# Kernel tuning notes

Measured on AMD Instinct MI355X. Metric: run time of the kernel, lower is better.

The kernel has to match this reference:

```python
import jax, jax.numpy as jnp
import numpy as np

EMBED_DIM = 768
NUM_HEADS = 12
HEAD_DIM = EMBED_DIM // NUM_HEADS


def setup_inputs() -> dict:
    key = jax.random.key(0)
    ks = jax.random.split(key, 9)
    s = 1.0 / np.sqrt(EMBED_DIM)
    inp = {
        "x": jax.random.normal(ks[0], (4, 2048, EMBED_DIM), dtype=jnp.float32),
        "W_q": jax.random.uniform(ks[1], (EMBED_DIM, EMBED_DIM), jnp.float32, -s, s),
        "b_q": jax.random.uniform(ks[2], (EMBED_DIM,), jnp.float32, -s, s),
        "W_k": jax.random.uniform(ks[3], (EMBED_DIM, EMBED_DIM), jnp.float32, -s, s),
        "b_k": jax.random.uniform(ks[4], (EMBED_DIM,), jnp.float32, -s, s),
        "W_v": jax.random.uniform(ks[5], (EMBED_DIM, EMBED_DIM), jnp.float32, -s, s),
        "b_v": jax.random.uniform(ks[6], (EMBED_DIM,), jnp.float32, -s, s),
        "W_out": jax.random.uniform(ks[7], (EMBED_DIM, EMBED_DIM), jnp.float32, -s, s),
        "b_out": jax.random.uniform(ks[8], (EMBED_DIM,), jnp.float32, -s, s),
    }
    return inp


def reference(x, W_q, b_q, W_k, b_k, W_v, b_v, W_out, b_out):
    B, N, D = x.shape
    H, Hd = NUM_HEADS, HEAD_DIM
    scale = 1.0 / jnp.sqrt(jnp.asarray(Hd, x.dtype))
    # QKV projections (torch Linear: x @ W.T + b)
    Q = (x @ W_q.T + b_q).reshape(B, N, H, Hd).transpose(0, 2, 1, 3)  # (B,H,N,Hd)
    K = (x @ W_k.T + b_k).reshape(B, N, H, Hd).transpose(0, 2, 1, 3)
    V = (x @ W_v.T + b_v).reshape(B, N, H, Hd).transpose(0, 2, 1, 3)
    scores = jnp.einsum("bhqd,bhkd->bhqk", Q, K) * scale  # (B,H,N,N)
    attn = jax.nn.softmax(scores, axis=-1)
    out = jnp.einsum("bhqk,bhkd->bhqd", attn, V)  # (B,H,N,Hd)
    out = out.transpose(0, 2, 1, 3).reshape(B, N, D)
    return out @ W_out.T + b_out
```

## Files before the change

### kernel.cpp

```cpp
#include <hip/hip_runtime.h>
#include <math.h>

#define D_EMB 768
#define SEQN 2048
#define NB 4
#define NH 12
#define HDIM 64
#define MTOT (NB*SEQN)
#define SCLQ 0.18033688011112042f

typedef unsigned int u32;
typedef unsigned short u16;
typedef short sh4 __attribute__((ext_vector_type(4)));
typedef short bf16x8 __attribute__((ext_vector_type(8)));
typedef float f32x16 __attribute__((ext_vector_type(16)));

#define MFMA32(a,b,c) __builtin_amdgcn_mfma_f32_32x32x16_bf16((a),(b),(c),0,0,0)

__device__ __forceinline__ u32 cvtpk(float a, float b){
    u32 r; asm("v_cvt_pk_bf16_f32 %0, %1, %2" : "=v"(r) : "v"(a), "v"(b)); return r;
}
__device__ __forceinline__ u32 pack_split(float v){
    u32 h = cvtpk(v, v);
    float hf = __builtin_bit_cast(float, h << 16);
    float r = v - hf;
    u32 l = cvtpk(r, r);
    return __builtin_amdgcn_perm(l, h, 0x05040100u);
}
__device__ __forceinline__ void unpack4(uint4 p, sh4& hi, sh4& lo){
    u32 h0 = __builtin_amdgcn_perm(p.y, p.x, 0x05040100u);
    u32 h1 = __builtin_amdgcn_perm(p.w, p.z, 0x05040100u);
    u32 l0 = __builtin_amdgcn_perm(p.y, p.x, 0x07060302u);
    u32 l1 = __builtin_amdgcn_perm(p.w, p.z, 0x07060302u);
    uint2 h = {h0, h1}, l = {l0, l1};
    hi = __builtin_bit_cast(sh4, h);
    lo = __builtin_bit_cast(sh4, l);
}
__device__ __forceinline__ bf16x8 ldfrag(const short* p){
    sh4 a = *(const sh4*)p;
    sh4 b = *(const sh4*)(p+4);
    return __builtin_shufflevector(a,b,0,1,2,3,4,5,6,7);
}

__global__ __launch_bounds__(256) void pack_bf(const float* __restrict__ s, u16* __restrict__ d, int n4){
    int i = blockIdx.x*256 + threadIdx.x;
    if (i >= n4) return;
    float4 v = ((const float4*)s)[i];
    uint2 o = { cvtpk(v.x, v.y), cvtpk(v.z, v.w) };
    ((uint2*)d)[i] = o;
}
__global__ __launch_bounds__(256) void pack_wbf(const float* __restrict__ w0, const float* __restrict__ w1,
                                                const float* __restrict__ w2, const float* __restrict__ w3,
                                                u16* __restrict__ d, int n4){
    const int z = blockIdx.y;
    const float* s = (z==0)?w0:(z==1)?w1:(z==2)?w2:w3;
    int i = blockIdx.x*256 + threadIdx.x;
    if (i >= n4) return;
    float4 v = ((const float4*)s)[i];
    uint2 o = { cvtpk(v.x, v.y), cvtpk(v.z, v.w) };
    ((uint2*)(d + (size_t)z*n4*4))[i] = o;
}

#define GPAD 36

__global__ __launch_bounds__(256,3) void gemm_qkv(const u16* __restrict__ X, const u16* __restrict__ Wb,
        const float* __restrict__ bq, const float* __restrict__ bk, const float* __restrict__ bv,
        u16* __restrict__ oq, u16* __restrict__ okk, u16* __restrict__ ov){
    __shared__ __align__(16) short Ahi[128][GPAD];
    __shared__ __align__(16) short Bhi[128][GPAD];

    const int tid = threadIdx.x;
    const int l = tid & 63, w = tid >> 6;
    const int lq = l & 31, g = l >> 5;
    const int wm = w >> 1, wn = w & 1;
    const int m0 = blockIdx.x * 128;
    const int n0 = blockIdx.y * 128;
    const int z  = blockIdx.z;
    const u16* W = Wb + (size_t)z * D_EMB * D_EMB;
    const float* bias = (z==0) ? bq : (z==1) ? bk : bv;
    u16* out = (z==0) ? oq : (z==1) ? okk : ov;

    f32x16 acc[2][2];
    #pragma unroll
    for (int i=0;i<2;i++)
        #pragma unroll
        for (int j=0;j<2;j++)
            #pragma unroll
            for (int r=0;r<16;r++) acc[i][j][r] = 0.f;

    const int srow = tid >> 1;
    const int skb  = (tid & 1) * 16;
    const u16* ap0 = X + (size_t)(m0+srow)*D_EMB + skb;
    const u16* wp0 = W + (size_t)(n0+srow)*D_EMB + skb;

    uint4 a0 = *(const uint4*)ap0, a1 = *(const uint4*)(ap0+8);
    uint4 w0 = *(const uint4*)wp0, w1 = *(const uint4*)(wp0+8);

    for (int k0 = 0; k0 < D_EMB; k0 += 32) {
        __syncthreads();
        {
            uint2 t;
            t.x=a0.x; t.y=a0.y; *(uint2*)&Ahi[srow][skb]    = t;
            t.x=a0.z; t.y=a0.w; *(uint2*)&Ahi[srow][skb+4]  = t;
            t.x=a1.x; t.y=a1.y; *(uint2*)&Ahi[srow][skb+8]  = t;
            t.x=a1.z; t.y=a1.w; *(uint2*)&Ahi[srow][skb+12] = t;
            t.x=w0.x; t.y=w0.y; *(uint2*)&Bhi[srow][skb]    = t;
            t.x=w0.z; t.y=w0.w; *(uint2*)&Bhi[srow][skb+4]  = t;
            t.x=w1.x; t.y=w1.y; *(uint2*)&Bhi[srow][skb+8]  = t;
            t.x=w1.z; t.y=w1.w; *(uint2*)&Bhi[srow][skb+12] = t;
        }
        if (k0 + 32 < D_EMB){
            const u16* ap = ap0 + k0 + 32;
            const u16* wp = wp0 + k0 + 32;
            a0 = *(const uint4*)ap; a1 = *(const uint4*)(ap+8);
            w0 = *(const uint4*)wp; w1 = *(const uint4*)(wp+8);
        }
        __syncthreads();
        #pragma unroll
        for (int kk=0;kk<2;kk++){
            const int kc = kk*16 + g*8;
            bf16x8 ah[2], bh[2];
            #pragma unroll
            for (int i=0;i<2;i++) ah[i] = ldfrag(&Ahi[wm*64+32*i+lq][kc]);
            #pragma unroll
            for (int j=0;j<2;j++) bh[j] = ldfrag(&Bhi[wn*64+32*j+lq][kc]);
            #pragma unroll
            for (int i=0;i<2;i++)
                #pragma unroll
                for (int j=0;j<2;j++)
                    acc[i][j] = MFMA32(ah[i], bh[j], acc[i][j]);
        }
    }

    #pragma unroll
    for (int j=0;j<2;j++){
        const int c = n0 + wn*64 + 32*j + lq;
        const float bv2 = bias[c];
        #pragma unroll
        for (int i=0;i<2;i++){
            #pragma unroll
            for (int r=0;r<16;r++){
                const int m = m0 + wm*64 + 32*i + (r&3) + 8*(r>>2) + 4*g;
                float v = acc[i][j][r] + bv2;
                if (z==0) v *= SCLQ;
                const int b = m >> 11, n = m & 2047, h = c >> 6, hd = c & 63;
                out[(((size_t)(b*NH + h))*SEQN + n)*HDIM + hd] = (u16)cvtpk(v, v);
            }
        }
    }
}

__global__ __launch_bounds__(256,3) void gemm_out(const u32* __restrict__ A, const u16* __restrict__ Wb,
        const float* __restrict__ bo, float* __restrict__ outp){
    __shared__ __align__(16) short Ahi[128][GPAD];
    __shared__ __align__(16) short Alo[128][GPAD];
    __shared__ __align__(16) short Bhi[128][GPAD];

    const int tid = threadIdx.x;
    const int l = tid & 63, w = tid >> 6;
    const int lq = l & 31, g = l >> 5;
    const int wm = w >> 1, wn = w & 1;
    const int m0 = blockIdx.x * 128;
    const int n0 = blockIdx.y * 128;
    const u16* W = Wb + (size_t)3 * D_EMB * D_EMB;

    f32x16 acc[2][2];
    #pragma unroll
    for (int i=0;i<2;i++)
        #pragma unroll
        for (int j=0;j<2;j++)
            #pragma unroll
            for (int r=0;r<16;r++) acc[i][j][r] = 0.f;

    const int srow = tid >> 1;
    const int skb  = (tid & 1) * 16;
    const u32* ap0 = A + (size_t)(m0+srow)*D_EMB + skb;
    const u16* wp0 = W + (size_t)(n0+srow)*D_EMB + skb;

    uint4 areg[4];
    uint4 w0 = *(const uint4*)wp0, w1 = *(const uint4*)(wp0+8);
    #pragma unroll
    for (int c=0;c<4;c++) areg[c] = *(const uint4*)(ap0 + 4*c);

    for (int k0 = 0; k0 < D_EMB; k0 += 32) {
        __syncthreads();
        #pragma unroll
        for (int c=0;c<4;c++){
            sh4 h, lo2; unpack4(areg[c], h, lo2);
            *(sh4*)&Ahi[srow][skb+4*c] = h;
            *(sh4*)&Alo[srow][skb+4*c] = lo2;
        }
        {
            uint2 t;
            t.x=w0.x; t.y=w0.y; *(uint2*)&Bhi[srow][skb]    = t;
            t.x=w0.z; t.y=w0.w; *(uint2*)&Bhi[srow][skb+4]  = t;
            t.x=w1.x; t.y=w1.y; *(uint2*)&Bhi[srow][skb+8]  = t;
            t.x=w1.z; t.y=w1.w; *(uint2*)&Bhi[srow][skb+12] = t;
        }
        if (k0 + 32 < D_EMB){
            const u32* ap = ap0 + k0 + 32;
            const u16* wp = wp0 + k0 + 32;
            #pragma unroll
            for (int c=0;c<4;c++) areg[c] = *(const uint4*)(ap + 4*c);
            w0 = *(const uint4*)wp; w1 = *(const uint4*)(wp+8);
        }
        __syncthreads();
        #pragma unroll
        for (int kk=0;kk<2;kk++){
            const int kc = kk*16 + g*8;
            bf16x8 ah[2], al[2], bh[2];
            #pragma unroll
            for (int i=0;i<2;i++){
                ah[i] = ldfrag(&Ahi[wm*64+32*i+lq][kc]);
                al[i] = ldfrag(&Alo[wm*64+32*i+lq][kc]);
            }
            #pragma unroll
            for (int j=0;j<2;j++) bh[j] = ldfrag(&Bhi[wn*64+32*j+lq][kc]);
            #pragma unroll
            for (int i=0;i<2;i++)
                #pragma unroll
                for (int j=0;j<2;j++){
                    acc[i][j] = MFMA32(ah[i], bh[j], acc[i][j]);
                    acc[i][j] = MFMA32(al[i], bh[j], acc[i][j]);
                }
        }
    }

    #pragma unroll
    for (int j=0;j<2;j++){
        const int c = n0 + wn*64 + 32*j + lq;
        const float bv2 = bo[c];
        #pragma unroll
        for (int i=0;i<2;i++){
            #pragma unroll
            for (int r=0;r<16;r++){
                const int m = m0 + wm*64 + 32*i + (r&3) + 8*(r>>2) + 4*g;
                outp[(size_t)m*D_EMB + c] = acc[i][j][r] + bv2;
            }
        }
    }
}

#define KB 64
#define KPAD 68
#define NT (SEQN/KB)

__global__ __launch_bounds__(256,3) void attn_bf(const u16* __restrict__ Qg,
                                                 const u16* __restrict__ Kg,
                                                 const u16* __restrict__ Vg,
                                                 u32* __restrict__ Og) {
    __shared__ __align__(16) short Khi[2][KB][KPAD];
    __shared__ __align__(16) short Vthi[2][HDIM][KPAD];

    const int tid = threadIdx.x;
    const int l = tid & 63, w = tid >> 6;
    const int lq = l & 31, g = l >> 5;
    const int qt = blockIdx.x;
    const int bh = blockIdx.y;
    const size_t base = (size_t)bh * SEQN * HDIM;
    const int qrow = qt*128 + w*32 + lq;

    const int key = tid >> 2, dblk = (tid & 3) * 16;
    const int hd = tid & 63, kg = tid >> 6;
    const u16* kp0 = Kg + base + (size_t)key*HDIM + dblk;
    const u16* vp0 = Vg + base + (size_t)(kg*16)*HDIM + hd;

    bf16x8 qh[4];
    {
        const u16* qp = Qg + base + (size_t)qrow*HDIM;
        #pragma unroll
        for (int kk=0;kk<4;kk++){
            uint4 a = *(const uint4*)(qp + kk*16 + g*8);
            qh[kk] = __builtin_bit_cast(bf16x8, a);
        }
    }

    f32x16 o0, o1, zro;
    #pragma unroll
    for (int r=0;r<16;r++){ o0[r]=0.f; o1[r]=0.f; zro[r]=0.f; }
    float2 lr2 = {0.f, 0.f};

    uint4 kra, krb;
    u32 vt[16];

    auto loadTile = [&](int t){
        const u16* kp = kp0 + (size_t)t*KB*HDIM;
        const u16* vp = vp0 + (size_t)t*KB*HDIM;
        kra = *(const uint4*)kp;
        krb = *(const uint4*)(kp+8);
        #pragma unroll
        for (int i2=0;i2<16;i2++) vt[i2] = vp[(size_t)i2*HDIM];
    };
    auto stageWrite = [&](int cb){
        uint2 t;
        t.x=kra.x; t.y=kra.y; *(uint2*)&Khi[cb][key][dblk]    = t;
        t.x=kra.z; t.y=kra.w; *(uint2*)&Khi[cb][key][dblk+4]  = t;
        t.x=krb.x; t.y=krb.y; *(uint2*)&Khi[cb][key][dblk+8]  = t;
        t.x=krb.z; t.y=krb.w; *(uint2*)&Khi[cb][key][dblk+12] = t;
        #pragma unroll
        for (int c=0;c<4;c++){
            uint2 v2;
            v2.x = __builtin_amdgcn_perm(vt[4*c+1], vt[4*c+0], 0x05040100u);
            v2.y = __builtin_amdgcn_perm(vt[4*c+3], vt[4*c+2], 0x05040100u);
            *(uint2*)&Vthi[cb][hd][kg*16+4*c] = v2;
        }
    };

    loadTile(0);
    stageWrite(0);
    loadTile(1);

    for (int kt=0; kt<NT; kt++){
        const int cb = kt & 1;
        __syncthreads();
        if (kt+1 < NT){
            stageWrite(cb^1);
            if (kt+2 < NT) loadTile(kt+2);
        }

        f32x16 s0, s1;
        __builtin_amdgcn_s_setprio(1);
        {
            bf16x8 a0h = ldfrag(&Khi[cb][lq][0 + g*8]);
            bf16x8 a1h = ldfrag(&Khi[cb][32+lq][0 + g*8]);
            s0 = MFMA32(a0h, qh[0], zro);
            s1 = MFMA32(a1h, qh[0], zro);
        }
        #pragma unroll
        for (int kk=1;kk<4;kk++){
            const int kc = kk*16 + g*8;
            bf16x8 a0h = ldfrag(&Khi[cb][lq][kc]);
            bf16x8 a1h = ldfrag(&Khi[cb][32+lq][kc]);
            s0 = MFMA32(a0h, qh[kk], s0);
            s1 = MFMA32(a1h, qh[kk], s1);
        }
        __builtin_amdgcn_s_setprio(0);

        #pragma unroll
        for (int r=0;r<16;r++) s0[r] = __builtin_amdgcn_exp2f(s0[r]);
        #pragma unroll
        for (int r=0;r<16;r++) s1[r] = __builtin_amdgcn_exp2f(s1[r]);
        #pragma unroll
        for (int r=0;r<16;r+=2){
            float2 a = {s0[r], s0[r+1]};
            float2 b = {s1[r], s1[r+1]};
            lr2 += a;
            lr2 += b;
        }

        u32 pk0h[8], pk1h[8];
        #pragma unroll
        for (int j=0;j<8;j++){
            pk0h[j] = cvtpk(s0[2*j], s0[2*j+1]);
            pk1h[j] = cvtpk(s1[2*j], s1[2*j+1]);
        }
        u32 n0[2][4], n1[2][4];
        #pragma unroll
        for (int a2=0;a2<2;a2++){
            #pragma unroll
            for (int c=0;c<2;c++){
                u32 x0 = pk0h[4*a2+c], y0 = pk0h[4*a2+2+c];
                asm("v_permlane32_swap_b32 %0, %1" : "+v"(x0), "+v"(y0));
                n0[0][2*a2+c] = x0; n1[0][2*a2+c] = y0;
                u32 x1 = pk1h[4*a2+c], y1 = pk1h[4*a2+2+c];
                asm("v_permlane32_swap_b32 %0, %1" : "+v"(x1), "+v"(y1));
                n0[1][2*a2+c] = x1; n1[1][2*a2+c] = y1;
            }
        }

        __builtin_amdgcn_s_setprio(1);
        #pragma unroll
        for (int kk=0;kk<4;kk++){
            const int hblk = kk>>1, a2 = kk&1;
            uint4 whv = { n0[hblk][2*a2], n0[hblk][2*a2+1], n1[hblk][2*a2], n1[hblk][2*a2+1] };
            bf16x8 pbh = __builtin_bit_cast(bf16x8, whv);
            const int kc = kk*16 + g*8;
            bf16x8 v0h = ldfrag(&Vthi[cb][lq][kc]);
            bf16x8 v1h = ldfrag(&Vthi[cb][32+lq][kc]);
            o0 = MFMA32(v0h, pbh, o0);
            o1 = MFMA32(v1h, pbh, o1);
        }
        __builtin_amdgcn_s_setprio(0);
    }

    float l_run = lr2.x + lr2.y;
    l_run += __shfl_xor(l_run, 32);
    const float inv = 1.f / l_run;
    const int b = bh / NH, h = bh % NH;
    u32* op = Og + ((size_t)(b*SEQN + qrow))*D_EMB + h*HDIM;
    #pragma unroll
    for (int rq=0; rq<4; rq++){
        uint4 w0, w1;
        w0.x = pack_split(o0[4*rq+0]*inv); w0.y = pack_split(o0[4*rq+1]*inv);
        w0.z = pack_split(o0[4*rq+2]*inv); w0.w = pack_split(o0[4*rq+3]*inv);
        w1.x = pack_split(o1[4*rq+0]*inv); w1.y = pack_split(o1[4*rq+1]*inv);
        w1.z = pack_split(o1[4*rq+2]*inv); w1.w = pack_split(o1[4*rq+3]*inv);
        *(uint4*)(op + 8*rq + 4*g)      = w0;
        *(uint4*)(op + 32 + 8*rq + 4*g) = w1;
    }
}

extern "C" void kernel_launch(void* const* d_in, const int* in_sizes, int n_in,
                              void* d_out, int out_size, void* d_ws, size_t ws_size,
                              hipStream_t stream) {
    const float* x  = (const float*)d_in[0];
    const float* Wq = (const float*)d_in[1];
    const float* bq = (const float*)d_in[2];
    const float* Wk = (const float*)d_in[3];
    const float* bk = (const float*)d_in[4];
    const float* Wv = (const float*)d_in[5];
    const float* bv = (const float*)d_in[6];
    const float* Wo = (const float*)d_in[7];
    const float* bo = (const float*)d_in[8];

    const size_t per = (size_t)NB*NH*SEQN*HDIM;
    const size_t wplane = (size_t)D_EMB*D_EMB;
    u16* base16 = (u16*)d_ws;
    u16* Xbf = base16;
    u16* Qb  = base16 + per;
    u16* Kb  = base16 + 2*per;
    u16* Vb  = base16 + 3*per;
    u16* Wbf = base16 + 4*per;
    u32* ATpk = (u32*)(base16 + 4*per + 4*wplane);

    pack_bf<<<dim3((int)(per/4/256)), dim3(256), 0, stream>>>(x, Xbf, (int)(per/4));
    pack_wbf<<<dim3(576,4), dim3(256), 0, stream>>>(Wq, Wk, Wv, Wo, Wbf, (int)(wplane/4));

    gemm_qkv<<<dim3(MTOT/128, D_EMB/128, 3), dim3(256), 0, stream>>>(Xbf, Wbf, bq, bk, bv, Qb, Kb, Vb);

    attn_bf<<<dim3(SEQN/128, NB*NH), dim3(256), 0, stream>>>(Qb, Kb, Vb, ATpk);

    gemm_out<<<dim3(MTOT/128, D_EMB/128), dim3(256), 0, stream>>>(ATpk, Wbf, bo, (float*)d_out);
}
```

Measured before the change: 156.8 us.

## Fuse fp32-to-bf16 packing into GEMMs and load K fragments directly to registers

Removes the separate pack_bf and pack_wbf kernels; the QKV and output GEMMs now load fp32 X and weights and convert to bf16 while staging into LDS. This drops two launches and a round trip of the converted tensors through global memory, at the cost of twice the global bytes per tile inside the GEMMs. Separately, the attention kernel stops staging K in LDS and loads each lane's MFMA K fragments straight from global memory into registers, prefetching the next tile after the QK MFMAs. That frees LDS and removes LDS writes and reads, but uses more registers and issues less coalesced global loads.

```diff
diff --git a/kernel.cpp b/kernel.cpp
--- a/kernel.cpp
+++ b/kernel.cpp
@@ -42,28 +42,10 @@
     return __builtin_shufflevector(a,b,0,1,2,3,4,5,6,7);
 }
 
-__global__ __launch_bounds__(256) void pack_bf(const float* __restrict__ s, u16* __restrict__ d, int n4){
-    int i = blockIdx.x*256 + threadIdx.x;
-    if (i >= n4) return;
-    float4 v = ((const float4*)s)[i];
-    uint2 o = { cvtpk(v.x, v.y), cvtpk(v.z, v.w) };
-    ((uint2*)d)[i] = o;
-}
-__global__ __launch_bounds__(256) void pack_wbf(const float* __restrict__ w0, const float* __restrict__ w1,
-                                                const float* __restrict__ w2, const float* __restrict__ w3,
-                                                u16* __restrict__ d, int n4){
-    const int z = blockIdx.y;
-    const float* s = (z==0)?w0:(z==1)?w1:(z==2)?w2:w3;
-    int i = blockIdx.x*256 + threadIdx.x;
-    if (i >= n4) return;
-    float4 v = ((const float4*)s)[i];
-    uint2 o = { cvtpk(v.x, v.y), cvtpk(v.z, v.w) };
-    ((uint2*)(d + (size_t)z*n4*4))[i] = o;
-}
-
 #define GPAD 36
 
-__global__ __launch_bounds__(256,3) void gemm_qkv(const u16* __restrict__ X, const u16* __restrict__ Wb,
+__global__ __launch_bounds__(256,3) void gemm_qkv(const float* __restrict__ X,
+        const float* __restrict__ Wq, const float* __restrict__ Wk, const float* __restrict__ Wv,
         const float* __restrict__ bq, const float* __restrict__ bk, const float* __restrict__ bv,
         u16* __restrict__ oq, u16* __restrict__ okk, u16* __restrict__ ov){
     __shared__ __align__(16) short Ahi[128][GPAD];
@@ -76,7 +58,7 @@
     const int m0 = blockIdx.x * 128;
     const int n0 = blockIdx.y * 128;
     const int z  = blockIdx.z;
-    const u16* W = Wb + (size_t)z * D_EMB * D_EMB;
+    const float* W = (z==0) ? Wq : (z==1) ? Wk : Wv;
     const float* bias = (z==0) ? bq : (z==1) ? bk : bv;
     u16* out = (z==0) ? oq : (z==1) ? okk : ov;
 
@@ -90,30 +72,28 @@
 
     const int srow = tid >> 1;
     const int skb  = (tid & 1) * 16;
-    const u16* ap0 = X + (size_t)(m0+srow)*D_EMB + skb;
-    const u16* wp0 = W + (size_t)(n0+srow)*D_EMB + skb;
-
-    uint4 a0 = *(const uint4*)ap0, a1 = *(const uint4*)(ap0+8);
-    uint4 w0 = *(const uint4*)wp0, w1 = *(const uint4*)(wp0+8);
+    const float* ap0 = X + (size_t)(m0+srow)*D_EMB + skb;
+    const float* wp0 = W + (size_t)(n0+srow)*D_EMB + skb;
+
+    float4 ar[4], wr[4];
+    #pragma unroll
+    for (int c=0;c<4;c++){ ar[c] = *(const float4*)(ap0 + 4*c); wr[c] = *(const float4*)(wp0 + 4*c); }
 
     for (int k0 = 0; k0 < D_EMB; k0 += 32) {
         __syncthreads();
-        {
+        #pragma unroll
+        for (int c=0;c<4;c++){
             uint2 t;
-            t.x=a0.x; t.y=a0.y; *(uint2*)&Ahi[srow][skb]    = t;
-            t.x=a0.z; t.y=a0.w; *(uint2*)&Ahi[srow][skb+4]  = t;
-            t.x=a1.x; t.y=a1.y; *(uint2*)&Ahi[srow][skb+8]  = t;
-            t.x=a1.z; t.y=a1.w; *(uint2*)&Ahi[srow][skb+12] = t;
-            t.x=w0.x; t.y=w0.y; *(uint2*)&Bhi[srow][skb]    = t;
-            t.x=w0.z; t.y=w0.w; *(uint2*)&Bhi[srow][skb+4]  = t;
-            t.x=w1.x; t.y=w1.y; *(uint2*)&Bhi[srow][skb+8]  = t;
-            t.x=w1.z; t.y=w1.w; *(uint2*)&Bhi[srow][skb+12] = t;
+            t.x = cvtpk(ar[c].x, ar[c].y); t.y = cvtpk(ar[c].z, ar[c].w);
+            *(uint2*)&Ahi[srow][skb+4*c] = t;
+            t.x = cvtpk(wr[c].x, wr[c].y); t.y = cvtpk(wr[c].z, wr[c].w);
+            *(uint2*)&Bhi[srow][skb+4*c] = t;
         }
         if (k0 + 32 < D_EMB){
-            const u16* ap = ap0 + k0 + 32;
-            const u16* wp = wp0 + k0 + 32;
-            a0 = *(const uint4*)ap; a1 = *(const uint4*)(ap+8);
-            w0 = *(const uint4*)wp; w1 = *(const uint4*)(wp+8);
+            const float* ap = ap0 + k0 + 32;
+            const float* wp = wp0 + k0 + 32;
+            #pragma unroll
+            for (int c=0;c<4;c++){ ar[c] = *(const float4*)(ap + 4*c); wr[c] = *(const float4*)(wp + 4*c); }
         }
         __syncthreads();
         #pragma unroll
@@ -150,7 +130,7 @@
     }
 }
 
-__global__ __launch_bounds__(256,3) void gemm_out(const u32* __restrict__ A, const u16* __restrict__ Wb,
+__global__ __launch_bounds__(256,3) void gemm_out(const u32* __restrict__ A, const float* __restrict__ Wo,
         const float* __restrict__ bo, float* __restrict__ outp){
     __shared__ __align__(16) short Ahi[128][GPAD];
     __shared__ __align__(16) short Alo[128][GPAD];
@@ -162,7 +142,6 @@
     const int wm = w >> 1, wn = w & 1;
     const int m0 = blockIdx.x * 128;
     const int n0 = blockIdx.y * 128;
-    const u16* W = Wb + (size_t)3 * D_EMB * D_EMB;
 
     f32x16 acc[2][2];
     #pragma unroll
@@ -175,12 +154,12 @@
     const int srow = tid >> 1;
     const int skb  = (tid & 1) * 16;
     const u32* ap0 = A + (size_t)(m0+srow)*D_EMB + skb;
-    const u16* wp0 = W + (size_t)(n0+srow)*D_EMB + skb;
+    const float* wp0 = Wo + (size_t)(n0+srow)*D_EMB + skb;
 
     uint4 areg[4];
-    uint4 w0 = *(const uint4*)wp0, w1 = *(const uint4*)(wp0+8);
-    #pragma unroll
-    for (int c=0;c<4;c++) areg[c] = *(const uint4*)(ap0 + 4*c);
+    float4 wr[4];
+    #pragma unroll
+    for (int c=0;c<4;c++){ areg[c] = *(const uint4*)(ap0 + 4*c); wr[c] = *(const float4*)(wp0 + 4*c); }
 
     for (int k0 = 0; k0 < D_EMB; k0 += 32) {
         __syncthreads();
@@ -189,20 +168,15 @@
             sh4 h, lo2; unpack4(areg[c], h, lo2);
             *(sh4*)&Ahi[srow][skb+4*c] = h;
             *(sh4*)&Alo[srow][skb+4*c] = lo2;
-        }
-        {
             uint2 t;
-            t.x=w0.x; t.y=w0.y; *(uint2*)&Bhi[srow][skb]    = t;
-            t.x=w0.z; t.y=w0.w; *(uint2*)&Bhi[srow][skb+4]  = t;
-            t.x=w1.x; t.y=w1.y; *(uint2*)&Bhi[srow][skb+8]  = t;
-            t.x=w1.z; t.y=w1.w; *(uint2*)&Bhi[srow][skb+12] = t;
+            t.x = cvtpk(wr[c].x, wr[c].y); t.y = cvtpk(wr[c].z, wr[c].w);
+            *(uint2*)&Bhi[srow][skb+4*c] = t;
         }
         if (k0 + 32 < D_EMB){
             const u32* ap = ap0 + k0 + 32;
-            const u16* wp = wp0 + k0 + 32;
-            #pragma unroll
-            for (int c=0;c<4;c++) areg[c] = *(const uint4*)(ap + 4*c);
-            w0 = *(const uint4*)wp; w1 = *(const uint4*)(wp+8);
+            const float* wp = wp0 + k0 + 32;
+            #pragma unroll
+            for (int c=0;c<4;c++){ areg[c] = *(const uint4*)(ap + 4*c); wr[c] = *(const float4*)(wp + 4*c); }
         }
         __syncthreads();
         #pragma unroll
@@ -249,7 +223,6 @@
                                                  const u16* __restrict__ Kg,
                                                  const u16* __restrict__ Vg,
                                                  u32* __restrict__ Og) {
-    __shared__ __align__(16) short Khi[2][KB][KPAD];
     __shared__ __align__(16) short Vthi[2][HDIM][KPAD];
 
     const int tid = threadIdx.x;
@@ -260,10 +233,9 @@
     const size_t base = (size_t)bh * SEQN * HDIM;
     const int qrow = qt*128 + w*32 + lq;
 
-    const int key = tid >> 2, dblk = (tid & 3) * 16;
     const int hd = tid & 63, kg = tid >> 6;
-    const u16* kp0 = Kg + base + (size_t)key*HDIM + dblk;
     const u16* vp0 = Vg + base + (size_t)(kg*16)*HDIM + hd;
+    const u16* kfl = Kg + base + (size_t)lq*HDIM + g*8;
 
     bf16x8 qh[4];
     {
@@ -280,23 +252,15 @@
     for (int r=0;r<16;r++){ o0[r]=0.f; o1[r]=0.f; zro[r]=0.f; }
     float2 lr2 = {0.f, 0.f};
 
-    uint4 kra, krb;
     u32 vt[16];
-
-    auto loadTile = [&](int t){
-        const u16* kp = kp0 + (size_t)t*KB*HDIM;
+    uint4 kreg[8];
+
+    auto loadV = [&](int t){
         const u16* vp = vp0 + (size_t)t*KB*HDIM;
-        kra = *(const uint4*)kp;
-        krb = *(const uint4*)(kp+8);
         #pragma unroll
         for (int i2=0;i2<16;i2++) vt[i2] = vp[(size_t)i2*HDIM];
     };
-    auto stageWrite = [&](int cb){
-        uint2 t;
-        t.x=kra.x; t.y=kra.y; *(uint2*)&Khi[cb][key][dblk]    = t;
-        t.x=kra.z; t.y=kra.w; *(uint2*)&Khi[cb][key][dblk+4]  = t;
-        t.x=krb.x; t.y=krb.y; *(uint2*)&Khi[cb][key][dblk+8]  = t;
-        t.x=krb.z; t.y=krb.w; *(uint2*)&Khi[cb][key][dblk+12] = t;
+    auto stageV = [&](int cb){
         #pragma unroll
         for (int c=0;c<4;c++){
             uint2 v2;
@@ -305,36 +269,39 @@
             *(uint2*)&Vthi[cb][hd][kg*16+4*c] = v2;
         }
     };
-
-    loadTile(0);
-    stageWrite(0);
-    loadTile(1);
+    auto loadK = [&](int t){
+        const u16* kp = kfl + (size_t)t*KB*HDIM;
+        #pragma unroll
+        for (int blk=0;blk<2;blk++)
+            #pragma unroll
+            for (int kk=0;kk<4;kk++)
+                kreg[blk*4+kk] = *(const uint4*)(kp + blk*32*HDIM + kk*16);
+    };
+
+    loadK(0);
+    loadV(0);
+    stageV(0);
+    loadV(1);
 
     for (int kt=0; kt<NT; kt++){
         const int cb = kt & 1;
         __syncthreads();
         if (kt+1 < NT){
-            stageWrite(cb^1);
-            if (kt+2 < NT) loadTile(kt+2);
+            stageV(cb^1);
+            if (kt+2 < NT) loadV(kt+2);
         }
 
         f32x16 s0, s1;
         __builtin_amdgcn_s_setprio(1);
-        {
-            bf16x8 a0h = ldfrag(&Khi[cb][lq][0 + g*8]);
-            bf16x8 a1h = ldfrag(&Khi[cb][32+lq][0 + g*8]);
-            s0 = MFMA32(a0h, qh[0], zro);
-            s1 = MFMA32(a1h, qh[0], zro);
-        }
+        s0 = MFMA32(__builtin_bit_cast(bf16x8, kreg[0]), qh[0], zro);
+        s1 = MFMA32(__builtin_bit_cast(bf16x8, kreg[4]), qh[0], zro);
         #pragma unroll
         for (int kk=1;kk<4;kk++){
-            const int kc = kk*16 + g*8;
-            bf16x8 a0h = ldfrag(&Khi[cb][lq][kc]);
-            bf16x8 a1h = ldfrag(&Khi[cb][32+lq][kc]);
-            s0 = MFMA32(a0h, qh[kk], s0);
-            s1 = MFMA32(a1h, qh[kk], s1);
+            s0 = MFMA32(__builtin_bit_cast(bf16x8, kreg[kk]),   qh[kk], s0);
+            s1 = MFMA32(__builtin_bit_cast(bf16x8, kreg[4+kk]), qh[kk], s1);
         }
         __builtin_amdgcn_s_setprio(0);
+        if (kt+1 < NT) loadK(kt+1);
 
         #pragma unroll
         for (int r=0;r<16;r++) s0[r] = __builtin_amdgcn_exp2f(s0[r]);
@@ -414,21 +381,15 @@
     const float* bo = (const float*)d_in[8];
 
     const size_t per = (size_t)NB*NH*SEQN*HDIM;
-    const size_t wplane = (size_t)D_EMB*D_EMB;
     u16* base16 = (u16*)d_ws;
-    u16* Xbf = base16;
-    u16* Qb  = base16 + per;
-    u16* Kb  = base16 + 2*per;
-    u16* Vb  = base16 + 3*per;
-    u16* Wbf = base16 + 4*per;
-    u32* ATpk = (u32*)(base16 + 4*per + 4*wplane);
-
-    pack_bf<<<dim3((int)(per/4/256)), dim3(256), 0, stream>>>(x, Xbf, (int)(per/4));
-    pack_wbf<<<dim3(576,4), dim3(256), 0, stream>>>(Wq, Wk, Wv, Wo, Wbf, (int)(wplane/4));
-
-    gemm_qkv<<<dim3(MTOT/128, D_EMB/128, 3), dim3(256), 0, stream>>>(Xbf, Wbf, bq, bk, bv, Qb, Kb, Vb);
+    u16* Qb  = base16;
+    u16* Kb  = base16 + per;
+    u16* Vb  = base16 + 2*per;
+    u32* ATpk = (u32*)(base16 + 4*per);
+
+    gemm_qkv<<<dim3(MTOT/128, D_EMB/128, 3), dim3(256), 0, stream>>>(x, Wq, Wk, Wv, bq, bk, bv, Qb, Kb, Vb);
 
     attn_bf<<<dim3(SEQN/128, NB*NH), dim3(256), 0, stream>>>(Qb, Kb, Vb, ATpk);
 
-    gemm_out<<<dim3(MTOT/128, D_EMB/128), dim3(256), 0, stream>>>(ATpk, Wbf, bo, (float*)d_out);
-}
+    gemm_out<<<dim3(MTOT/128, D_EMB/128), dim3(256), 0, stream>>>(ATpk, Wo, bo, (float*)d_out);
+}
```

Measured after the change: 204.7 us. 30.5% more time.

## Process two query tiles per wave in attention to reuse K/V fragments

Applied to the files above, without the earlier changes.

Each wave in the attention kernel now handles 64 query rows as two 32-row groups instead of one. Every K and V fragment read from LDS therefore feeds twice as many MFMAs, and the grid is halved so each block covers 256 queries. Staging K/V into shared memory is amortised over more queries, and LDS read traffic per unit of work drops. The cost is higher register pressure: launch bounds drop from 3 to 2 blocks per CU, and fewer blocks (384) are launched, which may reduce occupancy and latency hiding.

```diff
diff --git a/kernel.cpp b/kernel.cpp
--- a/kernel.cpp
+++ b/kernel.cpp
@@ -245,7 +245,7 @@
 #define KPAD 68
 #define NT (SEQN/KB)
 
-__global__ __launch_bounds__(256,3) void attn_bf(const u16* __restrict__ Qg,
+__global__ __launch_bounds__(256,2) void attn_bf(const u16* __restrict__ Qg,
                                                  const u16* __restrict__ Kg,
                                                  const u16* __restrict__ Vg,
                                                  u32* __restrict__ Og) {
@@ -258,27 +258,29 @@
     const int qt = blockIdx.x;
     const int bh = blockIdx.y;
     const size_t base = (size_t)bh * SEQN * HDIM;
-    const int qrow = qt*128 + w*32 + lq;
+    const int qrowA = qt*256 + w*64 + lq;
+    const int qrowB = qrowA + 32;
 
     const int key = tid >> 2, dblk = (tid & 3) * 16;
     const int hd = tid & 63, kg = tid >> 6;
     const u16* kp0 = Kg + base + (size_t)key*HDIM + dblk;
     const u16* vp0 = Vg + base + (size_t)(kg*16)*HDIM + hd;
 
-    bf16x8 qh[4];
+    bf16x8 qhA[4], qhB[4];
     {
-        const u16* qp = Qg + base + (size_t)qrow*HDIM;
+        const u16* qpA = Qg + base + (size_t)qrowA*HDIM;
+        const u16* qpB = Qg + base + (size_t)qrowB*HDIM;
         #pragma unroll
         for (int kk=0;kk<4;kk++){
-            uint4 a = *(const uint4*)(qp + kk*16 + g*8);
-            qh[kk] = __builtin_bit_cast(bf16x8, a);
-        }
-    }
-
-    f32x16 o0, o1, zro;
-    #pragma unroll
-    for (int r=0;r<16;r++){ o0[r]=0.f; o1[r]=0.f; zro[r]=0.f; }
-    float2 lr2 = {0.f, 0.f};
+            qhA[kk] = __builtin_bit_cast(bf16x8, *(const uint4*)(qpA + kk*16 + g*8));
+            qhB[kk] = __builtin_bit_cast(bf16x8, *(const uint4*)(qpB + kk*16 + g*8));
+        }
+    }
+
+    f32x16 oA0, oA1, oB0, oB1, zro;
+    #pragma unroll
+    for (int r=0;r<16;r++){ oA0[r]=0.f; oA1[r]=0.f; oB0[r]=0.f; oB1[r]=0.f; zro[r]=0.f; }
+    float2 lrA = {0.f, 0.f}, lrB = {0.f, 0.f};
 
     uint4 kra, krb;
     u32 vt[16];
@@ -318,85 +320,105 @@
             if (kt+2 < NT) loadTile(kt+2);
         }
 
-        f32x16 s0, s1;
-        __builtin_amdgcn_s_setprio(1);
-        {
-            bf16x8 a0h = ldfrag(&Khi[cb][lq][0 + g*8]);
-            bf16x8 a1h = ldfrag(&Khi[cb][32+lq][0 + g*8]);
-            s0 = MFMA32(a0h, qh[0], zro);
-            s1 = MFMA32(a1h, qh[0], zro);
-        }
-        #pragma unroll
-        for (int kk=1;kk<4;kk++){
-            const int kc = kk*16 + g*8;
-            bf16x8 a0h = ldfrag(&Khi[cb][lq][kc]);
-            bf16x8 a1h = ldfrag(&Khi[cb][32+lq][kc]);
-            s0 = MFMA32(a0h, qh[kk], s0);
-            s1 = MFMA32(a1h, qh[kk], s1);
-        }
-        __builtin_amdgcn_s_setprio(0);
-
-        #pragma unroll
-        for (int r=0;r<16;r++) s0[r] = __builtin_amdgcn_exp2f(s0[r]);
-        #pragma unroll
-        for (int r=0;r<16;r++) s1[r] = __builtin_amdgcn_exp2f(s1[r]);
-        #pragma unroll
-        for (int r=0;r<16;r+=2){
-            float2 a = {s0[r], s0[r+1]};
-            float2 b = {s1[r], s1[r+1]};
-            lr2 += a;
-            lr2 += b;
-        }
-
-        u32 pk0h[8], pk1h[8];
-        #pragma unroll
-        for (int j=0;j<8;j++){
-            pk0h[j] = cvtpk(s0[2*j], s0[2*j+1]);
-            pk1h[j] = cvtpk(s1[2*j], s1[2*j+1]);
-        }
-        u32 n0[2][4], n1[2][4];
-        #pragma unroll
-        for (int a2=0;a2<2;a2++){
-            #pragma unroll
-            for (int c=0;c<2;c++){
-                u32 x0 = pk0h[4*a2+c], y0 = pk0h[4*a2+2+c];
-                asm("v_permlane32_swap_b32 %0, %1" : "+v"(x0), "+v"(y0));
-                n0[0][2*a2+c] = x0; n1[0][2*a2+c] = y0;
-                u32 x1 = pk1h[4*a2+c], y1 = pk1h[4*a2+2+c];
-                asm("v_permlane32_swap_b32 %0, %1" : "+v"(x1), "+v"(y1));
-                n0[1][2*a2+c] = x1; n1[1][2*a2+c] = y1;
-            }
-        }
-
-        __builtin_amdgcn_s_setprio(1);
-        #pragma unroll
-        for (int kk=0;kk<4;kk++){
-            const int hblk = kk>>1, a2 = kk&1;
-            uint4 whv = { n0[hblk][2*a2], n0[hblk][2*a2+1], n1[hblk][2*a2], n1[hblk][2*a2+1] };
-            bf16x8 pbh = __builtin_bit_cast(bf16x8, whv);
-            const int kc = kk*16 + g*8;
-            bf16x8 v0h = ldfrag(&Vthi[cb][lq][kc]);
-            bf16x8 v1h = ldfrag(&Vthi[cb][32+lq][kc]);
-            o0 = MFMA32(v0h, pbh, o0);
-            o1 = MFMA32(v1h, pbh, o1);
-        }
-        __builtin_amdgcn_s_setprio(0);
-    }
-
-    float l_run = lr2.x + lr2.y;
-    l_run += __shfl_xor(l_run, 32);
-    const float inv = 1.f / l_run;
+        #pragma unroll
+        for (int kb=0; kb<2; kb++){
+            f32x16 sA, sB;
+            __builtin_amdgcn_s_setprio(1);
+            {
+                bf16x8 a = ldfrag(&Khi[cb][kb*32+lq][g*8]);
+                sA = MFMA32(a, qhA[0], zro);
+                sB = MFMA32(a, qhB[0], zro);
+            }
+            #pragma unroll
+            for (int kk=1;kk<4;kk++){
+                bf16x8 a = ldfrag(&Khi[cb][kb*32+lq][kk*16 + g*8]);
+                sA = MFMA32(a, qhA[kk], sA);
+                sB = MFMA32(a, qhB[kk], sB);
+            }
+            __builtin_amdgcn_s_setprio(0);
+
+            #pragma unroll
+            for (int r=0;r<16;r++){ sA[r] = __builtin_amdgcn_exp2f(sA[r]); sB[r] = __builtin_amdgcn_exp2f(sB[r]); }
+            #pragma unroll
+            for (int r=0;r<16;r+=2){
+                float2 a2 = {sA[r], sA[r+1]};
+                float2 b2 = {sB[r], sB[r+1]};
+                lrA += a2;
+                lrB += b2;
+            }
+
+            u32 pkA[8], pkB[8];
+            #pragma unroll
+            for (int j=0;j<8;j++){
+                pkA[j] = cvtpk(sA[2*j], sA[2*j+1]);
+                pkB[j] = cvtpk(sB[2*j], sB[2*j+1]);
+            }
+            u32 nA0[4], nA1[4], nB0[4], nB1[4];
+            #pragma unroll
+            for (int a2=0;a2<2;a2++){
+                #pragma unroll
+                for (int c=0;c<2;c++){
+                    u32 x0 = pkA[4*a2+c], y0 = pkA[4*a2+2+c];
+                    asm("v_permlane32_swap_b32 %0, %1" : "+v"(x0), "+v"(y0));
+                    nA0[2*a2+c] = x0; nA1[2*a2+c] = y0;
+                    u32 x1 = pkB[4*a2+c], y1 = pkB[4*a2+2+c];
+                    asm("v_permlane32_swap_b32 %0, %1" : "+v"(x1), "+v"(y1));
+                    nB0[2*a2+c] = x1; nB1[2*a2+c] = y1;
+                }
+            }
+
+            __builtin_amdgcn_s_setprio(1);
+            #pragma unroll
+            for (int t2=0; t2<2; t2++){
+                const int kk = 2*kb + t2;
+                uint4 wAv = { nA0[2*t2], nA0[2*t2+1], nA1[2*t2], nA1[2*t2+1] };
+                uint4 wBv = { nB0[2*t2], nB0[2*t2+1], nB1[2*t2], nB1[2*t2+1] };
+                bf16x8 pbA = __builtin_bit_cast(bf16x8, wAv);
+                bf16x8 pbB = __builtin_bit_cast(bf16x8, wBv);
+                const int kc = kk*16 + g*8;
+                bf16x8 v0h = ldfrag(&Vthi[cb][lq][kc]);
+                bf16x8 v1h = ldfrag(&Vthi[cb][32+lq][kc]);
+                oA0 = MFMA32(v0h, pbA, oA0);
+                oA1 = MFMA32(v1h, pbA, oA1);
+                oB0 = MFMA32(v0h, pbB, oB0);
+                oB1 = MFMA32(v1h, pbB, oB1);
+            }
+            __builtin_amdgcn_s_setprio(0);
+        }
+    }
+
     const int b = bh / NH, h = bh % NH;
-    u32* op = Og + ((size_t)(b*SEQN + qrow))*D_EMB + h*HDIM;
-    #pragma unroll
-    for (int rq=0; rq<4; rq++){
-        uint4 w0, w1;
-        w0.x = pack_split(o0[4*rq+0]*inv); w0.y = pack_split(o0[4*rq+1]*inv);
-        w0.z = pack_split(o0[4*rq+2]*inv); w0.w = pack_split(o0[4*rq+3]*inv);
-        w1.x = pack_split(o1[4*rq+0]*inv); w1.y = pack_split(o1[4*rq+1]*inv);
-        w1.z = pack_split(o1[4*rq+2]*inv); w1.w = pack_split(o1[4*rq+3]*inv);
-        *(uint4*)(op + 8*rq + 4*g)      = w0;
-        *(uint4*)(op + 32 + 8*rq + 4*g) = w1;
+    {
+        float lA = lrA.x + lrA.y;
+        lA += __shfl_xor(lA, 32);
+        const float inv = 1.f / lA;
+        u32* op = Og + ((size_t)(b*SEQN + qrowA))*D_EMB + h*HDIM;
+        #pragma unroll
+        for (int rq=0; rq<4; rq++){
+            uint4 w0, w1;
+            w0.x = pack_split(oA0[4*rq+0]*inv); w0.y = pack_split(oA0[4*rq+1]*inv);
+            w0.z = pack_split(oA0[4*rq+2]*inv); w0.w = pack_split(oA0[4*rq+3]*inv);
+            w1.x = pack_split(oA1[4*rq+0]*inv); w1.y = pack_split(oA1[4*rq+1]*inv);
+            w1.z = pack_split(oA1[4*rq+2]*inv); w1.w = pack_split(oA1[4*rq+3]*inv);
+            *(uint4*)(op + 8*rq + 4*g)      = w0;
+            *(uint4*)(op + 32 + 8*rq + 4*g) = w1;
+        }
+    }
+    {
+        float lB = lrB.x + lrB.y;
+        lB += __shfl_xor(lB, 32);
+        const float inv = 1.f / lB;
+        u32* op = Og + ((size_t)(b*SEQN + qrowB))*D_EMB + h*HDIM;
+        #pragma unroll
+        for (int rq=0; rq<4; rq++){
+            uint4 w0, w1;
+            w0.x = pack_split(oB0[4*rq+0]*inv); w0.y = pack_split(oB0[4*rq+1]*inv);
+            w0.z = pack_split(oB0[4*rq+2]*inv); w0.w = pack_split(oB0[4*rq+3]*inv);
+            w1.x = pack_split(oB1[4*rq+0]*inv); w1.y = pack_split(oB1[4*rq+1]*inv);
+            w1.z = pack_split(oB1[4*rq+2]*inv); w1.w = pack_split(oB1[4*rq+3]*inv);
+            *(uint4*)(op + 8*rq + 4*g)      = w0;
+            *(uint4*)(op + 32 + 8*rq + 4*g) = w1;
+        }
     }
 }
 
@@ -428,7 +450,7 @@
 
     gemm_qkv<<<dim3(MTOT/128, D_EMB/128, 3), dim3(256), 0, stream>>>(Xbf, Wbf, bq, bk, bv, Qb, Kb, Vb);
 
-    attn_bf<<<dim3(SEQN/128, NB*NH), dim3(256), 0, stream>>>(Qb, Kb, Vb, ATpk);
+    attn_bf<<<dim3(SEQN/256, NB*NH), dim3(256), 0, stream>>>(Qb, Kb, Vb, ATpk);
 
     gemm_out<<<dim3(MTOT/128, D_EMB/128), dim3(256), 0, stream>>>(ATpk, Wbf, bo, (float*)d_out);
 }
```

New measurement: 165.1 us. +5.3%, slower.
